# Kernel tuning notes

Hardware: AMD Instinct MI355X
Metric: run time of the kernel (lower is better)

The kernel has to match this reference:

```python
import jax, jax.numpy as jnp
import numpy as np

B, C, I, DI, DO = 256, 10, 1152, 8, 16  # batch, classes, in_caps, in_dim, out_dim
N_ITERS = 3


def _squash(s):
    # s: [..., DO]; scale = |s|^2/(1+|s|^2) * 1/|s|
    sq = jnp.sum(s * s, axis=-1, keepdims=True)
    return (sq / (1.0 + sq)) * s / jnp.sqrt(sq)


def setup_inputs() -> dict:
    key = jax.random.key(0)
    kx, kw = jax.random.split(key)
    x = jax.random.normal(kx, (B, I, DI), dtype=jnp.float32)
    # learned prediction weights: [num_classes, in_caps, out_caps=1, out_dim, in_dim]
    W = jax.random.normal(kw, (C, I, 1, DO, DI), dtype=jnp.float32)
    return {"x": x, "W": W}


def reference(x, W):
    # prediction vectors u_hat[b,c,i,:] = W[c,i] @ x[b,i]  -> [B, C, I, DO]
    u_hat = jnp.einsum('cidk,bik->bcid', W[:, :, 0], x)
    # routing logits b: [B, C, I, 1]
    blog = jnp.zeros(u_hat.shape[:3] + (1,), dtype=u_hat.dtype)
    v = None
    for it in range(N_ITERS):
        c = jax.nn.softmax(blog, axis=1)                 # softmax over classes
        s = jnp.sum(c * u_hat, axis=2, keepdims=True)    # [B, C, 1, DO]
        v = _squash(s)                                   # [B, C, 1, DO]
        if it != N_ITERS - 1:
            # agreement: <u_hat[b,c,i,:], v[b,c,0,:]> -> [B, C, I, 1]
            blog = blog + jnp.sum(u_hat * v, axis=-1, keepdims=True)
    return v  # [B, C, 1, DO]
```

## Files before the change

kernel.cpp:

```cpp
#include <hip/hip_runtime.h>


#define NCLS   10
#define NCAPS  1152
#define KDO    16
#define CHUNK  128
#define NCH    9
#define NB     256
#define BBAT   8

typedef _Float16 h2_t __attribute__((ext_vector_type(2)));
typedef unsigned u4 __attribute__((ext_vector_type(4)));

static __device__ __forceinline__ unsigned pack2h(float a, float b) {
    union { _Float16 h[2]; unsigned u; } p;
    p.h[0] = (_Float16)a;
    p.h[1] = (_Float16)b;
    return p.u;
}

static __device__ __forceinline__ float dot8h(u4 r, const unsigned* xh) {
    union { unsigned u; h2_t h; } w0, w1, w2, w3, a0, a1, a2, a3;
    w0.u = r.x; w1.u = r.y; w2.u = r.z; w3.u = r.w;
    a0.u = xh[0]; a1.u = xh[1]; a2.u = xh[2]; a3.u = xh[3];
#if __has_builtin(__builtin_amdgcn_fdot2)
    float acc = __builtin_amdgcn_fdot2(w0.h, a0.h, 0.f, false);
    acc = __builtin_amdgcn_fdot2(w1.h, a1.h, acc, false);
    acc = __builtin_amdgcn_fdot2(w2.h, a2.h, acc, false);
    acc = __builtin_amdgcn_fdot2(w3.h, a3.h, acc, false);
    return acc;
#else
    return (float)w0.h.x * (float)a0.h.x + (float)w0.h.y * (float)a0.h.y
         + (float)w1.h.x * (float)a1.h.x + (float)w1.h.y * (float)a1.h.y
         + (float)w2.h.x * (float)a2.h.x + (float)w2.h.y * (float)a2.h.y
         + (float)w3.h.x * (float)a3.h.x + (float)w3.h.y * (float)a3.h.y;
#endif
}

static __device__ __forceinline__ float dot2h(unsigned a, unsigned b, float acc) {
    union { unsigned u; h2_t h; } pa, pb;
    pa.u = a; pb.u = b;
#if __has_builtin(__builtin_amdgcn_fdot2)
    return __builtin_amdgcn_fdot2(pa.h, pb.h, acc, false);
#else
    return acc + (float)pa.h.x * (float)pb.h.x + (float)pa.h.y * (float)pb.h.y;
#endif
}

static __device__ __forceinline__ float bfly16(const float v[KDO], int lane) {
    float a[8];
    #pragma unroll
    for (int i = 0; i < 8; ++i) {
        float send = (lane & 32) ? v[i] : v[i + 8];
        float recv = __shfl_xor(send, 32, 64);
        float keep = (lane & 32) ? v[i + 8] : v[i];
        a[i] = keep + recv;
    }
    float b[4];
    #pragma unroll
    for (int i = 0; i < 4; ++i) {
        float send = (lane & 16) ? a[i] : a[i + 4];
        float recv = __shfl_xor(send, 16, 64);
        float keep = (lane & 16) ? a[i + 4] : a[i];
        b[i] = keep + recv;
    }
    float c[2];
    #pragma unroll
    for (int i = 0; i < 2; ++i) {
        float send = (lane & 8) ? b[i] : b[i + 2];
        float recv = __shfl_xor(send, 8, 64);
        float keep = (lane & 8) ? b[i + 2] : b[i];
        c[i] = keep + recv;
    }
    float e;
    {
        float send = (lane & 4) ? c[0] : c[1];
        float recv = __shfl_xor(send, 4, 64);
        float keep = (lane & 4) ? c[1] : c[0];
        e = keep + recv;
    }
    e += __shfl_xor(e, 2, 64);
    e += __shfl_xor(e, 1, 64);
    return e;
}

static __device__ __forceinline__ int bfly_d(int lane) {
    return ((lane & 4) ? 1 : 0) | ((lane & 8) ? 2 : 0)
         | ((lane & 16) ? 4 : 0) | ((lane & 32) ? 8 : 0);
}

__global__ __launch_bounds__(256)
void k_pack(const float4* __restrict__ W4, u4* __restrict__ Wt,
            const float4* __restrict__ x4, u4* __restrict__ xp) {
    int bid = blockIdx.x;
    if (bid < 720) {
        int tid = bid * 256 + threadIdx.x;
        int d = tid & 15;
        int rest = tid >> 4;
        int i = rest % NCAPS;
        int c = rest / NCAPS;
        float4 a = W4[2 * tid];
        float4 b = W4[2 * tid + 1];
        u4 o;
        o.x = pack2h(a.x, a.y);
        o.y = pack2h(a.z, a.w);
        o.z = pack2h(b.x, b.y);
        o.w = pack2h(b.z, b.w);
        Wt[(size_t)(c * KDO + d) * NCAPS + i] = o;
    } else {
        int tid = (bid - 720) * 256 + threadIdx.x;
        float4 a = x4[2 * tid];
        float4 b = x4[2 * tid + 1];
        u4 o;
        o.x = pack2h(a.x, a.y);
        o.y = pack2h(a.z, a.w);
        o.z = pack2h(b.x, b.y);
        o.w = pack2h(b.z, b.w);
        xp[tid] = o;
    }
}

__global__ __launch_bounds__(CHUNK, 1)
void k_uhat(const u4* __restrict__ Wt, const u4* __restrict__ xp,
            u4* __restrict__ ut, float* __restrict__ psum)
{
    __shared__ float red0[2][BBAT][KDO];
    const int t    = threadIdx.x;
    const int lane = t & 63;
    const int wave = t >> 6;
    const int ii = blockIdx.x * CHUNK + t;
    const int b0 = blockIdx.y * BBAT;
    const int c  = blockIdx.z;
    const int dm = bfly_d(lane);

    u4 xq[BBAT];
    #pragma unroll
    for (int k = 0; k < BBAT; ++k)
        xq[k] = xp[(size_t)(b0 + k) * NCAPS + ii];

    const u4* base = Wt + (size_t)c * KDO * NCAPS + ii;
    u4 r[KDO];
    #pragma unroll
    for (int d = 0; d < KDO; ++d)
        r[d] = base[(size_t)d * NCAPS];

    #pragma unroll
    for (int k = 0; k < BBAT; ++k) {
        const unsigned* xh = (const unsigned*)&xq[k];
        u4 h0, h1;
        float sacc[KDO];
        #pragma unroll
        for (int dp = 0; dp < 8; ++dp) {
            float u0 = dot8h(r[2 * dp],     xh);
            float u1 = dot8h(r[2 * dp + 1], xh);
            sacc[2 * dp]     = u0;
            sacc[2 * dp + 1] = u1;
            unsigned pk = pack2h(u0, u1);
            if (dp < 4) ((unsigned*)&h0)[dp] = pk;
            else        ((unsigned*)&h1)[dp - 4] = pk;
        }
        u4* utb = ut + (size_t)(b0 + k) * NCLS * 2 * NCAPS;
        utb[((size_t)c * 2 + 0) * NCAPS + ii] = h0;
        utb[((size_t)c * 2 + 1) * NCAPS + ii] = h1;

        float e = bfly16(sacc, lane);
        if ((lane & 3) == 0) red0[wave][k][dm] = e;
    }
    __syncthreads();
    {
        int k = t >> 4, d = t & 15;
        float v = red0[0][k][d] + red0[1][k][d];
        psum[(((size_t)(b0 + k) * NCH + blockIdx.x) * NCLS + c) * KDO + d] = v;
    }
}

__global__ __launch_bounds__(CHUNK, 1)
void k_iter(const u4* __restrict__ ut,
            const float* __restrict__ psA, float scaleA,
            const float* __restrict__ psB,
            float* __restrict__ psOut)
{
    __shared__ __align__(16) float s0sh[NCLS * KDO];
    __shared__ __align__(16) float s1sh[NCLS * KDO];
    __shared__ float scsh[2][NCLS];
    __shared__ unsigned vsh[NCLS * 8];
    __shared__ float red[2][NCLS * KDO];
    const int t    = threadIdx.x;
    const int lane = t & 63;
    const int wave = t >> 6;
    const int ii = blockIdx.x * CHUNK + t;
    const int b  = blockIdx.y;
    const int dm = bfly_d(lane);

    if (t < 40) {
        const float4* pA4 = (const float4*)psA + (size_t)b * NCH * 40;
        float4 s = {0.f, 0.f, 0.f, 0.f};
        #pragma unroll
        for (int ch = 0; ch < NCH; ++ch) {
            float4 v = pA4[ch * 40 + t];
            s.x += v.x; s.y += v.y; s.z += v.z; s.w += v.w;
        }
        float4 o = {s.x * scaleA, s.y * scaleA, s.z * scaleA, s.w * scaleA};
        ((float4*)s0sh)[t] = o;
    } else if (psB && t >= 64 && t < 104) {
        const int j = t - 64;
        const float4* pB4 = (const float4*)psB + (size_t)b * NCH * 40;
        float4 s = {0.f, 0.f, 0.f, 0.f};
        #pragma unroll
        for (int ch = 0; ch < NCH; ++ch) {
            float4 v = pB4[ch * 40 + j];
            s.x += v.x; s.y += v.y; s.z += v.z; s.w += v.w;
        }
        ((float4*)s1sh)[j] = s;
    }
    __syncthreads();
    if (t < (psB ? 2 * NCLS : NCLS)) {
        int which = t >= NCLS;
        int c = which ? t - NCLS : t;
        const float* ss = which ? s1sh : s0sh;
        float nsq = 0.f;
        #pragma unroll
        for (int d = 0; d < KDO; ++d) {
            float x = ss[c * KDO + d];
            nsq += x * x;
        }
        scsh[which][c] = sqrtf(nsq) / (1.f + nsq);
    }
    __syncthreads();
    if (t < NCLS * 8) {
        int c = t >> 3, dp = t & 7;
        float va = s0sh[c * KDO + 2 * dp]     * scsh[0][c];
        float vb = s0sh[c * KDO + 2 * dp + 1] * scsh[0][c];
        if (psB) {
            va += s1sh[c * KDO + 2 * dp]     * scsh[1][c];
            vb += s1sh[c * KDO + 2 * dp + 1] * scsh[1][c];
        }
        vsh[t] = pack2h(va, vb);
    }
    __syncthreads();

    const u4* utb = ut + (size_t)b * NCLS * 2 * NCAPS;

    u4 up0[NCLS], up1[NCLS];
    #pragma unroll
    for (int c = 0; c < NCLS; ++c) {
        up0[c] = utb[((size_t)c * 2 + 0) * NCAPS + ii];
        up1[c] = utb[((size_t)c * 2 + 1) * NCAPS + ii];
    }

    float bl[NCLS];
    #pragma unroll
    for (int c = 0; c < NCLS; ++c) {
        float a = 0.f;
        #pragma unroll
        for (int dp = 0; dp < 4; ++dp)
            a = dot2h(((const unsigned*)&up0[c])[dp], vsh[c * 8 + dp], a);
        #pragma unroll
        for (int dp = 0; dp < 4; ++dp)
            a = dot2h(((const unsigned*)&up1[c])[dp], vsh[c * 8 + 4 + dp], a);
        bl[c] = a;
    }

    float m = bl[0];
    #pragma unroll
    for (int c = 1; c < NCLS; ++c) m = fmaxf(m, bl[c]);
    float den = 0.f;
    #pragma unroll
    for (int c = 0; c < NCLS; ++c) den += __expf(bl[c] - m);
    float sid = 1.f / den;
    #pragma unroll
    for (int c = 0; c < NCLS; ++c) bl[c] = __expf(bl[c] - m) * sid;

    #pragma unroll
    for (int c = 0; c < NCLS; ++c) {
        float sacc[KDO];
        #pragma unroll
        for (int dp = 0; dp < 8; ++dp) {
            union { unsigned u; h2_t h; } p;
            p.u = (dp < 4) ? ((const unsigned*)&up0[c])[dp]
                           : ((const unsigned*)&up1[c])[dp - 4];
            sacc[2 * dp]     = bl[c] * (float)p.h.x;
            sacc[2 * dp + 1] = bl[c] * (float)p.h.y;
        }
        float e = bfly16(sacc, lane);
        if ((lane & 3) == 0) red[wave][c * KDO + dm] = e;
    }
    __syncthreads();
    if (t < 40) {
        float4 o;
        o.x = red[0][4 * t + 0] + red[1][4 * t + 0];
        o.y = red[0][4 * t + 1] + red[1][4 * t + 1];
        o.z = red[0][4 * t + 2] + red[1][4 * t + 2];
        o.w = red[0][4 * t + 3] + red[1][4 * t + 3];
        ((float4*)(psOut + ((size_t)b * NCH + blockIdx.x) * (NCLS * KDO)))[t] = o;
    }
}

__global__ __launch_bounds__(160)
void k_squash(const float* __restrict__ psum, float* __restrict__ out)
{
    __shared__ __align__(16) float ssh[NCLS * KDO];
    const int b = blockIdx.x;
    const int t = threadIdx.x;

    if (t < 40) {
        const float4* p4 = (const float4*)psum + (size_t)b * NCH * 40;
        float4 s = {0.f, 0.f, 0.f, 0.f};
        #pragma unroll
        for (int ch = 0; ch < NCH; ++ch) {
            float4 v = p4[ch * 40 + t];
            s.x += v.x; s.y += v.y; s.z += v.z; s.w += v.w;
        }
        ((float4*)ssh)[t] = s;
    }
    __syncthreads();
    if (t >= NCLS * KDO) return;

    float s = ssh[t];
    float nsq = s * s;
    nsq += __shfl_xor(nsq, 8, 16);
    nsq += __shfl_xor(nsq, 4, 16);
    nsq += __shfl_xor(nsq, 2, 16);
    nsq += __shfl_xor(nsq, 1, 16);
    float sc = sqrtf(nsq) / (1.f + nsq);
    out[(size_t)b * NCLS * KDO + t] = s * sc;
}

__global__ __launch_bounds__(256, 2)
void caps_routing_fb(const float* __restrict__ x, const float* __restrict__ W,
                     float* __restrict__ out)
{
    const int b    = blockIdx.x;
    const int t    = threadIdx.x;
    const int lane = t & 63;
    const int wave = t >> 6;
    __shared__ float v_prev[NCLS * KDO];
    __shared__ float redf[NCLS * 4 * KDO];
    float4 xr[5][2];
    const float4* x4 = reinterpret_cast<const float4*>(x + (size_t)b * NCAPS * 8);
    #pragma unroll
    for (int j = 0; j < 5; ++j) {
        int i = t + 256 * j;
        if (i < NCAPS) { xr[j][0] = x4[2 * i]; xr[j][1] = x4[2 * i + 1]; }
    }
    float blog[5][NCLS];
    #pragma unroll
    for (int j = 0; j < 5; ++j)
        #pragma unroll
        for (int c = 0; c < NCLS; ++c) blog[j][c] = 0.f;
    const float4* W4 = reinterpret_cast<const float4*>(W);
    for (int it = 0; it < 3; ++it) {
        if (it > 0) {
            for (int c = 0; c < NCLS; ++c) {
                float vp[KDO];
                #pragma unroll
                for (int d = 0; d < KDO; ++d) vp[d] = v_prev[c * KDO + d];
                #pragma unroll
                for (int j = 0; j < 5; ++j) {
                    int i = t + 256 * j;
                    if (i < NCAPS) {
                        size_t wbx = (size_t)(c * NCAPS + i) * 32;
                        float a = 0.f;
                        #pragma unroll
                        for (int d = 0; d < KDO; ++d) {
                            float4 w0 = W4[wbx + 2 * d]; float4 w1 = W4[wbx + 2 * d + 1];
                            float u = w0.x*xr[j][0].x + w0.y*xr[j][0].y + w0.z*xr[j][0].z
                                    + w0.w*xr[j][0].w + w1.x*xr[j][1].x + w1.y*xr[j][1].y
                                    + w1.z*xr[j][1].z + w1.w*xr[j][1].w;
                            a += u * vp[d];
                        }
                        blog[j][c] += a;
                    }
                }
            }
        }
        float sm2[5], sid2[5];
        #pragma unroll
        for (int j = 0; j < 5; ++j) {
            int i = t + 256 * j;
            if (i < NCAPS) {
                float m = blog[j][0];
                #pragma unroll
                for (int c = 1; c < NCLS; ++c) m = fmaxf(m, blog[j][c]);
                float den = 0.f;
                #pragma unroll
                for (int c = 0; c < NCLS; ++c) den += __expf(blog[j][c] - m);
                sm2[j] = m; sid2[j] = 1.f / den;
            }
        }
        for (int c = 0; c < NCLS; ++c) {
            float acc[KDO];
            #pragma unroll
            for (int d = 0; d < KDO; ++d) acc[d] = 0.f;
            #pragma unroll
            for (int j = 0; j < 5; ++j) {
                int i = t + 256 * j;
                if (i < NCAPS) {
                    float wq = __expf(blog[j][c] - sm2[j]) * sid2[j];
                    size_t wbx = (size_t)(c * NCAPS + i) * 32;
                    #pragma unroll
                    for (int d = 0; d < KDO; ++d) {
                        float4 w0 = W4[wbx + 2 * d]; float4 w1 = W4[wbx + 2 * d + 1];
                        float u = w0.x*xr[j][0].x + w0.y*xr[j][0].y + w0.z*xr[j][0].z
                                + w0.w*xr[j][0].w + w1.x*xr[j][1].x + w1.y*xr[j][1].y
                                + w1.z*xr[j][1].z + w1.w*xr[j][1].w;
                        acc[d] += wq * u;
                    }
                }
            }
            #pragma unroll
            for (int d = 0; d < KDO; ++d) {
                float v = acc[d];
                v += __shfl_xor(v, 32, 64); v += __shfl_xor(v, 16, 64);
                v += __shfl_xor(v,  8, 64); v += __shfl_xor(v,  4, 64);
                v += __shfl_xor(v,  2, 64); v += __shfl_xor(v,  1, 64);
                if (lane == 0) redf[(c * 4 + wave) * KDO + d] = v;
            }
        }
        __syncthreads();
        if (t < NCLS * KDO) {
            int c = t >> 4, d = t & 15;
            float s = redf[(c*4+0)*KDO+d] + redf[(c*4+1)*KDO+d]
                    + redf[(c*4+2)*KDO+d] + redf[(c*4+3)*KDO+d];
            float nsq = s * s;
            nsq += __shfl_xor(nsq, 8, 16); nsq += __shfl_xor(nsq, 4, 16);
            nsq += __shfl_xor(nsq, 2, 16); nsq += __shfl_xor(nsq, 1, 16);
            float scale = sqrtf(nsq) / (1.f + nsq);
            float vv = s * scale;
            v_prev[t] = vv;
            if (it == 2) out[(size_t)b * NCLS * KDO + t] = vv;
        }
        __syncthreads();
    }
}

extern "C" void kernel_launch(void* const* d_in, const int* in_sizes, int n_in,
                              void* d_out, int out_size, void* d_ws, size_t ws_size,
                              hipStream_t stream) {
    const float* x = (const float*)d_in[0];
    const float4* W4 = (const float4*)d_in[1];
    float* out = (float*)d_out;
    (void)in_sizes; (void)n_in; (void)out_size;

    const size_t WT = (size_t)NCLS * KDO * NCAPS * sizeof(u4);
    const size_t XH = (size_t)NB * NCAPS * sizeof(u4);
    const size_t UT = (size_t)NB * NCLS * 2 * NCAPS * sizeof(u4);
    const size_t PS = (size_t)NB * NCH * NCLS * KDO * sizeof(float);
    const size_t need = WT + XH + UT + 3 * PS;

    if (ws_size >= need) {
        char* p = (char*)d_ws;
        u4* Wt    = (u4*)p;    p += WT;
        u4* xp    = (u4*)p;    p += XH;
        u4* ut    = (u4*)p;    p += UT;
        float* ps0 = (float*)p; p += PS;
        float* ps1 = (float*)p; p += PS;
        float* ps2 = (float*)p;

        k_pack<<<dim3(720 + 1152), dim3(256), 0, stream>>>(
            W4, Wt, (const float4*)x, xp);
        k_uhat<<<dim3(NCH, NB / BBAT, NCLS), dim3(CHUNK), 0, stream>>>(
            Wt, xp, ut, ps0);
        k_iter<<<dim3(NCH, NB), dim3(CHUNK), 0, stream>>>(ut, ps0, 0.1f, nullptr, ps1);
        k_iter<<<dim3(NCH, NB), dim3(CHUNK), 0, stream>>>(ut, ps0, 0.1f, ps1, ps2);
        k_squash<<<dim3(NB), dim3(160), 0, stream>>>(ps2, out);
    } else {
        caps_routing_fb<<<dim3(NB), dim3(256), 0, stream>>>(x, (const float*)d_in[1], out);
    }
}
```

Before: 133.5 us.

## Split classes across wave pairs in routing iteration kernel

```diff
diff --git a/kernel.cpp b/kernel.cpp
--- a/kernel.cpp
+++ b/kernel.cpp
@@ -174,7 +174,7 @@
     }
 }
 
-__global__ __launch_bounds__(CHUNK, 1)
+__global__ __launch_bounds__(256)
 void k_iter(const u4* __restrict__ ut,
             const float* __restrict__ psA, float scaleA,
             const float* __restrict__ psB,
@@ -184,13 +184,18 @@
     __shared__ __align__(16) float s1sh[NCLS * KDO];
     __shared__ float scsh[2][NCLS];
     __shared__ unsigned vsh[NCLS * 8];
-    __shared__ float red[2][NCLS * KDO];
+    __shared__ float red[4][5 * KDO];
+    __shared__ float msh[256];
+    __shared__ float dsh[256];
     const int t    = threadIdx.x;
     const int lane = t & 63;
     const int wave = t >> 6;
-    const int ii = blockIdx.x * CHUNK + t;
-    const int b  = blockIdx.y;
-    const int dm = bfly_d(lane);
+    const int sub  = wave & 1;
+    const int half = wave >> 1;
+    const int c0   = half * 5;
+    const int ii   = blockIdx.x * CHUNK + sub * 64 + lane;
+    const int b    = blockIdx.y;
+    const int dm   = bfly_d(lane);
 
     if (t < 40) {
         const float4* pA4 = (const float4*)psA + (size_t)b * NCH * 40;
@@ -240,58 +245,66 @@
     __syncthreads();
 
     const u4* utb = ut + (size_t)b * NCLS * 2 * NCAPS;
-
-    u4 up0[NCLS], up1[NCLS];
-    #pragma unroll
-    for (int c = 0; c < NCLS; ++c) {
-        up0[c] = utb[((size_t)c * 2 + 0) * NCAPS + ii];
-        up1[c] = utb[((size_t)c * 2 + 1) * NCAPS + ii];
-    }
-
-    float bl[NCLS];
-    #pragma unroll
-    for (int c = 0; c < NCLS; ++c) {
+    u4 up0[5], up1[5];
+    #pragma unroll
+    for (int j = 0; j < 5; ++j) {
+        int c = c0 + j;
+        up0[j] = utb[((size_t)c * 2 + 0) * NCAPS + ii];
+        up1[j] = utb[((size_t)c * 2 + 1) * NCAPS + ii];
+    }
+
+    float bl[5];
+    #pragma unroll
+    for (int j = 0; j < 5; ++j) {
+        int c = c0 + j;
         float a = 0.f;
         #pragma unroll
         for (int dp = 0; dp < 4; ++dp)
-            a = dot2h(((const unsigned*)&up0[c])[dp], vsh[c * 8 + dp], a);
+            a = dot2h(((const unsigned*)&up0[j])[dp], vsh[c * 8 + dp], a);
         #pragma unroll
         for (int dp = 0; dp < 4; ++dp)
-            a = dot2h(((const unsigned*)&up1[c])[dp], vsh[c * 8 + 4 + dp], a);
-        bl[c] = a;
-    }
-
-    float m = bl[0];
-    #pragma unroll
-    for (int c = 1; c < NCLS; ++c) m = fmaxf(m, bl[c]);
-    float den = 0.f;
-    #pragma unroll
-    for (int c = 0; c < NCLS; ++c) den += __expf(bl[c] - m);
-    float sid = 1.f / den;
-    #pragma unroll
-    for (int c = 0; c < NCLS; ++c) bl[c] = __expf(bl[c] - m) * sid;
-
-    #pragma unroll
-    for (int c = 0; c < NCLS; ++c) {
+            a = dot2h(((const unsigned*)&up1[j])[dp], vsh[c * 8 + 4 + dp], a);
+        bl[j] = a;
+    }
+
+    float m5 = bl[0];
+    #pragma unroll
+    for (int j = 1; j < 5; ++j) m5 = fmaxf(m5, bl[j]);
+    msh[t] = m5;
+    __syncthreads();
+    float m = fmaxf(m5, msh[t ^ 128]);
+    float dp5 = 0.f;
+    #pragma unroll
+    for (int j = 0; j < 5; ++j) dp5 += __expf(bl[j] - m);
+    dsh[t] = dp5;
+    __syncthreads();
+    float sid = 1.f / (dp5 + dsh[t ^ 128]);
+    #pragma unroll
+    for (int j = 0; j < 5; ++j) bl[j] = __expf(bl[j] - m) * sid;
+
+    #pragma unroll
+    for (int j = 0; j < 5; ++j) {
         float sacc[KDO];
         #pragma unroll
         for (int dp = 0; dp < 8; ++dp) {
             union { unsigned u; h2_t h; } p;
-            p.u = (dp < 4) ? ((const unsigned*)&up0[c])[dp]
-                           : ((const unsigned*)&up1[c])[dp - 4];
-            sacc[2 * dp]     = bl[c] * (float)p.h.x;
-            sacc[2 * dp + 1] = bl[c] * (float)p.h.y;
+            p.u = (dp < 4) ? ((const unsigned*)&up0[j])[dp]
+                           : ((const unsigned*)&up1[j])[dp - 4];
+            sacc[2 * dp]     = bl[j] * (float)p.h.x;
+            sacc[2 * dp + 1] = bl[j] * (float)p.h.y;
         }
         float e = bfly16(sacc, lane);
-        if ((lane & 3) == 0) red[wave][c * KDO + dm] = e;
+        if ((lane & 3) == 0) red[wave][j * KDO + dm] = e;
     }
     __syncthreads();
     if (t < 40) {
+        int w0 = (t < 20) ? 0 : 2;
+        int ix = (t < 20) ? 4 * t : 4 * (t - 20);
         float4 o;
-        o.x = red[0][4 * t + 0] + red[1][4 * t + 0];
-        o.y = red[0][4 * t + 1] + red[1][4 * t + 1];
-        o.z = red[0][4 * t + 2] + red[1][4 * t + 2];
-        o.w = red[0][4 * t + 3] + red[1][4 * t + 3];
+        o.x = red[w0][ix + 0] + red[w0 + 1][ix + 0];
+        o.y = red[w0][ix + 1] + red[w0 + 1][ix + 1];
+        o.z = red[w0][ix + 2] + red[w0 + 1][ix + 2];
+        o.w = red[w0][ix + 3] + red[w0 + 1][ix + 3];
         ((float4*)(psOut + ((size_t)b * NCH + blockIdx.x) * (NCLS * KDO)))[t] = o;
     }
 }
@@ -461,8 +474,8 @@
             W4, Wt, (const float4*)x, xp);
         k_uhat<<<dim3(NCH, NB / BBAT, NCLS), dim3(CHUNK), 0, stream>>>(
             Wt, xp, ut, ps0);
-        k_iter<<<dim3(NCH, NB), dim3(CHUNK), 0, stream>>>(ut, ps0, 0.1f, nullptr, ps1);
-        k_iter<<<dim3(NCH, NB), dim3(CHUNK), 0, stream>>>(ut, ps0, 0.1f, ps1, ps2);
+        k_iter<<<dim3(NCH, NB), dim3(256), 0, stream>>>(ut, ps0, 0.1f, nullptr, ps1);
+        k_iter<<<dim3(NCH, NB), dim3(256), 0, stream>>>(ut, ps0, 0.1f, ps1, ps2);
         k_squash<<<dim3(NB), dim3(160), 0, stream>>>(ps2, out);
     } else {
         caps_routing_fb<<<dim3(NB), dim3(256), 0, stream>>>(x, (const float*)d_in[1], out);
```

Result: faster. 130.3 us, median of 2 (-2.4%).
